# Optimization experiments

Hardware: AMD Instinct MI355X
Metric: run time of the kernel (lower is better)

The kernel has to match this reference:

```python
import jax, jax.numpy as jnp
import numpy as np
from jax import lax

B, T, A, L, H, FD = 32, 64, 6, 32, 128, 256


def setup_inputs() -> dict:
    key = jax.random.key(0)
    ks = jax.random.split(key, 24)
    rn = lambda k, s, sc: jax.random.normal(k, s, jnp.float32) * sc
    return {
        "states": rn(ks[0], (B, T, 3, 64, 64), 1.0),
        "actions": rn(ks[1], (B, T, A), 1.0),
        # CNN encoder params (scale ~ 1/sqrt(fan_in))
        "c1_w": rn(ks[2], (32, 3, 4, 4), 0.14), "c1_b": rn(ks[3], (32,), 0.01),
        "c2_w": rn(ks[4], (64, 32, 4, 4), 0.044), "c2_b": rn(ks[5], (64,), 0.01),
        "c3_w": rn(ks[6], (128, 64, 4, 4), 0.031), "c3_b": rn(ks[7], (128,), 0.01),
        "c4_w": rn(ks[8], (256, 128, 4, 4), 0.022), "c4_b": rn(ks[9], (256,), 0.01),
        "fc_w": rn(ks[10], (FD, 256 * 4 * 4), 0.0156), "fc_b": rn(ks[11], (FD,), 0.01),
        # GRUCell params (torch layout: W_ih (3H, in), W_hh (3H, H))
        "gru_wih": rn(ks[12], (3 * H, L + A), 0.16), "gru_whh": rn(ks[13], (3 * H, H), 0.088),
        "gru_bih": rn(ks[14], (3 * H,), 0.01), "gru_bhh": rn(ks[15], (3 * H,), 0.01),
        "prior_w": rn(ks[16], (2 * L, H), 0.088), "prior_b": rn(ks[17], (2 * L,), 0.01),
        "post_w": rn(ks[18], (2 * L, H + FD), 0.05), "post_b": rn(ks[19], (2 * L,), 0.01),
        # reparameterization noise (randn_like in torch), one per (b, t)
        "eps": rn(ks[20], (B, T, L), 1.0),
    }


def _conv(x, w, b):
    # Conv2d(k=4, stride=2, pad=1), NCHW/OIHW
    y = lax.conv_general_dilated(x, w, window_strides=(2, 2),
                                 padding=[(1, 1), (1, 1)],
                                 dimension_numbers=("NCHW", "OIHW", "NCHW"))
    return jax.nn.relu(y + b[None, :, None, None])


def _encode(x, c1_w, c1_b, c2_w, c2_b, c3_w, c3_b, c4_w, c4_b, fc_w, fc_b):
    # x: (N, 3, 64, 64) -> (N, FD)
    x = _conv(x, c1_w, c1_b)
    x = _conv(x, c2_w, c2_b)
    x = _conv(x, c3_w, c3_b)
    x = _conv(x, c4_w, c4_b)  # (N, 256, 4, 4)
    x = x.reshape(x.shape[0], -1)
    return x @ fc_w.T + fc_b


def _gru_cell(x, h, wih, whh, bih, bhh):
    gi = x @ wih.T + bih
    gh = h @ whh.T + bhh
    i_r, i_z, i_n = jnp.split(gi, 3, axis=-1)
    h_r, h_z, h_n = jnp.split(gh, 3, axis=-1)
    r = jax.nn.sigmoid(i_r + h_r)
    z = jax.nn.sigmoid(i_z + h_z)
    n = jnp.tanh(i_n + r * h_n)
    return (1.0 - z) * n + z * h


def reference(states, actions, c1_w, c1_b, c2_w, c2_b, c3_w, c3_b, c4_w, c4_b,
              fc_w, fc_b, gru_wih, gru_whh, gru_bih, gru_bhh,
              prior_w, prior_b, post_w, post_b, eps):
    b, t = states.shape[0], states.shape[1]
    # encoder has no recurrent dependency: encode all frames at once
    feats = _encode(states.reshape(b * t, *states.shape[2:]),
                    c1_w, c1_b, c2_w, c2_b, c3_w, c3_b, c4_w, c4_b,
                    fc_w, fc_b).reshape(b, t, -1)  # (B, T, FD)

    def step(carry, inp):
        h, z = carry
        a_t, f_t, e_t = inp
        h = _gru_cell(jnp.concatenate([z, a_t], -1), h,
                      gru_wih, gru_whh, gru_bih, gru_bhh)
        mu_p, lv_p = jnp.split(h @ prior_w.T + prior_b, 2, axis=-1)
        mu_q, lv_q = jnp.split(jnp.concatenate([h, f_t], -1) @ post_w.T + post_b, 2, axis=-1)
        z = mu_q + jnp.exp(0.5 * lv_q) * e_t
        return (h, z), (mu_p, lv_p, mu_q, lv_q, h, z)

    h0 = jnp.zeros((b, gru_whh.shape[1]), states.dtype)
    z0 = jnp.zeros((b, prior_w.shape[0] // 2), states.dtype)
    xs = (jnp.swapaxes(actions, 0, 1), jnp.swapaxes(feats, 0, 1),
          jnp.swapaxes(eps, 0, 1))
    _, ys = lax.scan(step, (h0, z0), xs)
    # (T, B, d) -> (B, T, d)
    return tuple(jnp.swapaxes(y, 0, 1) for y in ys)
```

## Files before the change

kernel.cpp:

```cpp
#include <hip/hip_runtime.h>
#include <math.h>

#define Bn 32
#define Tn 64
#define An 6
#define Ln 32
#define Hn 128
#define FDn 256
#define Nimg (Bn*Tn)

typedef __attribute__((ext_vector_type(8))) short frag_ab;
typedef __attribute__((ext_vector_type(4))) float frag_cd;
typedef _Float16 h2_t __attribute__((ext_vector_type(2)));

__device__ __forceinline__ float sigmoid_fast(float x){
  return __builtin_amdgcn_rcpf(1.f + __expf(-x));
}
__device__ __forceinline__ float tanh_fast(float x){
  float x2 = fminf(fmaxf(2.f*x, -30.f), 30.f);
  float e = __expf(x2);
  return (e - 1.f) * __builtin_amdgcn_rcpf(e + 1.f);
}

__device__ __forceinline__ unsigned short f2bf(float f){
  unsigned int u = __float_as_uint(f);
  unsigned int r = (u + 0x7fffu + ((u >> 16) & 1u)) >> 16;
  return (unsigned short)r;
}
__device__ __forceinline__ unsigned packh(float a, float b){
  union { h2_t h; unsigned u; } x;
  x.h = (h2_t){(_Float16)a, (_Float16)b};
  return x.u;
}
__device__ __forceinline__ float fdot2u(unsigned a, unsigned b, float c){
  union { unsigned u; h2_t h; } ua, ub;
  ua.u = a; ub.u = b;
#if __has_builtin(__builtin_amdgcn_fdot2)
  return __builtin_amdgcn_fdot2(ua.h, ub.h, c, false);
#else
  return c + (float)ua.h.x*(float)ub.h.x + (float)ua.h.y*(float)ub.h.y;
#endif
}
#define BAR_LDS() asm volatile("s_waitcnt lgkmcnt(0)\n\ts_barrier" ::: "memory")

__device__ __forceinline__ int swz_w(int r, int p){
  return ((r >> 4) << 9) + (p << 7) + ((((r & 15) ^ (p << 2))) << 3);
}
__device__ __forceinline__ int swz_r(int f, int l){
  return (f << 9) + ((l >> 4) << 7) + ((((l & 15) ^ ((l >> 4) << 2))) << 3);
}

__global__ void __launch_bounds__(256)
states_nhwc_kernel(const float* __restrict__ src, unsigned short* __restrict__ dst)
{
  int idx = blockIdx.x*256 + threadIdx.x;
  int n = idx >> 12, pix = idx & 4095;
  const float* s = src + (size_t)n*3*4096 + pix;
  union { unsigned short e[4]; uint2 v; } u;
  u.e[0] = f2bf(s[0]); u.e[1] = f2bf(s[4096]); u.e[2] = f2bf(s[8192]); u.e[3] = 0;
  *(uint2*)(dst + (size_t)idx*4) = u.v;
}

#define WHH4_U 24576
#define PO4_U  (64*53*4)
#define SCAN_U (WHH4_U + PO4_U)

__global__ void __launch_bounds__(256)
prep2_kernel(const float* __restrict__ c1w, const float* __restrict__ c2w,
             const float* __restrict__ c3w, const float* __restrict__ c4w,
             const float* __restrict__ fcw,
             const float* __restrict__ gwhh, const float* __restrict__ gwih,
             const float* __restrict__ prw,  const float* __restrict__ pow_,
             unsigned short* __restrict__ w1p, unsigned short* __restrict__ w2p,
             unsigned short* __restrict__ w3p, unsigned short* __restrict__ w4p,
             unsigned short* __restrict__ wfcp,
             unsigned* __restrict__ g_scan, unsigned* __restrict__ g_wih2,
             unsigned* __restrict__ g_pr2)
{
  const int bid = blockIdx.x, tid = threadIdx.x;
  if (bid < 128){
    int idx = bid*256+tid;
    int k = idx >> 9, r = idx & 511, tap = r >> 5, c = r & 31;
    w2p[idx] = f2bf(c2w[k*512 + c*16 + tap]);
  } else if (bid < 640){
    int idx = (bid-128)*256+tid;
    int k = idx >> 10, r = idx & 1023, tap = r >> 6, c = r & 63;
    w3p[idx] = f2bf(c3w[k*1024 + c*16 + tap]);
  } else if (bid < 2688){
    int idx = (bid-640)*256+tid;
    int k = idx >> 11, r = idx & 2047, tap = r >> 7, c = r & 127;
    w4p[idx] = f2bf(c4w[k*2048 + c*16 + tap]);
  } else if (bid < 6784){
    int idx = (bid-2688)*256+tid;
    int o = idx >> 12, r = idx & 4095, sp = r >> 8, c = r & 255;
    wfcp[idx] = f2bf(fcw[o*4096 + c*16 + sp]);
  } else if (bid < 6792){
    int idx = (bid-6784)*256+tid;
    int k = idx >> 6, r = idx & 63, tap = r >> 2, c = r & 3;
    w1p[idx] = (c < 3) ? f2bf(c1w[k*48 + c*16 + tap]) : (unsigned short)0;
  } else if (bid < 6888){
    int idx = (bid-6792)*256+tid;
    int q = idx & 3, r2 = idx >> 2;
    int k8 = r2 / 384, i = r2 - k8*384;
    int k = 8*k8 + 2*q;
    g_scan[idx] = packh(gwhh[i*128 + k], gwhh[i*128 + k + 1]);
  } else if (bid < 6917){
    int idx = (bid-6888)*256+tid;
    if (idx < 19*384){
      int c = idx / 384, i = idx - c*384;
      g_wih2[idx] = packh(gwih[i*38 + 2*c], gwih[i*38 + 2*c + 1]);
    }
  } else if (bid < 6933){
    int idx = (bid-6917)*256+tid;
    int o = idx >> 6, c = idx & 63;
    g_pr2[idx] = packh(prw[o*128 + 2*c], prw[o*128 + 2*c + 1]);
  } else {
    int idx = (bid-6933)*256+tid;
    if (idx < 64*192){
      int o = idx / 192, r2 = idx - o*192;
      int u = r2 >> 2, q = r2 & 3;
      int j = u / 12, kk = u - j*12;
      int k = 96*j + 8*kk + 2*q;
      g_scan[WHH4_U + (o*53 + j*13 + kk)*4 + q] =
        packh(pow_[o*384 + k], pow_[o*384 + k + 1]);
    }
  }
}

template<int Cin, int IN, int Kout, int OUT, int BN, int LOG_SPB>
__global__ void __launch_bounds__(256)
convN_mfma(const unsigned short* __restrict__ in,
           const unsigned short* __restrict__ wB,
           const float* __restrict__ bias,
           unsigned short* __restrict__ out)
{
  constexpr int SPB = OUT*OUT;
  constexpr int KD  = 16*Cin;
  constexpr int NCH = KD/32;
  constexpr int NFN = BN/32;
  constexpr int BFR = BN/16;
  constexpr int BSL = (BN*4 + 255)/256;
  __shared__ __align__(16) unsigned short Alds[2][8*512];
  __shared__ __align__(16) unsigned short Blds[2][BFR*512];

  const int tid = threadIdx.x;
  const int wave = tid >> 6, lane = tid & 63;
  const unsigned m0 = blockIdx.x * 128;
  const int n0 = blockIdx.y * BN;

  const int p = tid & 3;
  const unsigned short* baseA[2]; int oyA[2], oxA[2]; int AdstI[2];
#pragma unroll
  for (int h = 0; h < 2; h++){
    int r = (tid >> 2) + h*64;
    unsigned m = m0 + r;
    int nimg = m >> LOG_SPB;
    int sp = m & (SPB - 1);
    oyA[h] = sp / OUT; oxA[h] = sp & (OUT - 1);
    baseA[h] = in + (size_t)nimg * IN * IN * Cin;
    AdstI[h] = swz_w(r, p);
  }

  const unsigned short* BsrcH[BSL]; int BdstIH[BSL]; bool bActH[BSL];
#pragma unroll
  for (int h = 0; h < BSL; h++){
    int bn = (tid >> 2) + h*64, pb = tid & 3;
    bActH[h] = bn < BN;
    BsrcH[h] = wB + (size_t)(n0 + bn)*KD + pb*8;
    BdstIH[h] = swz_w(bn, pb);
  }

  const int mhalf = wave >> 1, nhalf = wave & 1;
  frag_cd acc[4][NFN];
#pragma unroll
  for (int i = 0; i < 4; i++)
#pragma unroll
    for (int j = 0; j < NFN; j++) acc[i][j] = (frag_cd){0.f,0.f,0.f,0.f};

  auto loadA = [&](int kt, int h) -> uint4 {
    if constexpr (Cin >= 32){
      constexpr int CPT = Cin/32;
      int tap = kt / CPT;
      int c0 = (kt - tap*CPT)*32;
      int kh = tap >> 2, kw = tap & 3;
      int iy = 2*oyA[h] - 1 + kh;
      int ix = 2*oxA[h] - 1 + kw;
      uint4 v = {0u,0u,0u,0u};
      if ((unsigned)iy < (unsigned)IN && (unsigned)ix < (unsigned)IN)
        v = *(const uint4*)(baseA[h] + ((iy*IN + ix)*Cin + c0 + p*8));
      return v;
    } else {
      int kh = kt*2 + (p >> 1);
      int kw0 = (p & 1)*2;
      int iy = 2*oyA[h] - 1 + kh;
      int ix0 = 2*oxA[h] - 1 + kw0;
      union { uint2 u2[2]; uint4 u4; } v; v.u4 = (uint4){0u,0u,0u,0u};
      bool iyok = (unsigned)iy < (unsigned)IN;
      const unsigned short* rowp = baseA[h] + iy*IN*4;
#pragma unroll
      for (int d = 0; d < 2; d++){
        int ix = ix0 + d;
        if (iyok && (unsigned)ix < (unsigned)IN) v.u2[d] = *(const uint2*)(rowp + ix*4);
      }
      return v.u4;
    }
  };

  const int rdoff = swz_r(0, lane);

  uint4 aR0 = loadA(0,0), aR1 = loadA(0,1);
  uint4 bR[BSL];
#pragma unroll
  for (int h = 0; h < BSL; h++)
    bR[h] = bActH[h] ? *(const uint4*)BsrcH[h] : (uint4){0u,0u,0u,0u};
  *(uint4*)&Alds[0][AdstI[0]] = aR0;
  *(uint4*)&Alds[0][AdstI[1]] = aR1;
#pragma unroll
  for (int h = 0; h < BSL; h++)
    if (bActH[h]) *(uint4*)&Blds[0][BdstIH[h]] = bR[h];
  if (NCH > 1){
    aR0 = loadA(1,0); aR1 = loadA(1,1);
#pragma unroll
    for (int h = 0; h < BSL; h++)
      if (bActH[h]) bR[h] = *(const uint4*)(BsrcH[h] + 32);
  }
  BAR_LDS();

#pragma unroll 2
  for (int kt = 0; kt < NCH; kt++){
    const int cur = kt & 1, nxt = cur ^ 1;
    if (kt + 1 < NCH){
      *(uint4*)&Alds[nxt][AdstI[0]] = aR0;
      *(uint4*)&Alds[nxt][AdstI[1]] = aR1;
#pragma unroll
      for (int h = 0; h < BSL; h++)
        if (bActH[h]) *(uint4*)&Blds[nxt][BdstIH[h]] = bR[h];
      if (kt + 2 < NCH){
        aR0 = loadA(kt+2, 0);
        aR1 = loadA(kt+2, 1);
#pragma unroll
        for (int h = 0; h < BSL; h++)
          if (bActH[h]) bR[h] = *(const uint4*)(BsrcH[h] + (kt+2)*32);
      }
    }
    frag_ab a[4], bf[NFN];
#pragma unroll
    for (int i = 0; i < 4; i++)
      a[i] = *(const frag_ab*)&Alds[cur][(((mhalf<<2) + i) << 9) + rdoff];
#pragma unroll
    for (int j = 0; j < NFN; j++)
      bf[j] = *(const frag_ab*)&Blds[cur][((nhalf*NFN + j) << 9) + rdoff];
#pragma unroll
    for (int i = 0; i < 4; i++)
#pragma unroll
      for (int j = 0; j < NFN; j++)
        acc[i][j] = __builtin_amdgcn_mfma_f32_16x16x32_bf16(a[i], bf[j], acc[i][j], 0, 0, 0);
    BAR_LDS();
  }

  const unsigned mb = m0 + mhalf*64 + ((lane >> 4) << 2);
#pragma unroll
  for (int j = 0; j < NFN; j++){
    const int kg = n0 + nhalf*(NFN*16) + j*16 + (lane & 15);
    const float bv = bias[kg];
#pragma unroll
    for (int i = 0; i < 4; i++){
#pragma unroll
      for (int r = 0; r < 4; r++){
        unsigned mg = mb + i*16 + r;
        out[(size_t)mg*Kout + kg] = f2bf(fmaxf(acc[i][j][r] + bv, 0.f));
      }
    }
  }
}

__global__ void __launch_bounds__(256)
fc_mfma2(const unsigned short* __restrict__ A, const unsigned short* __restrict__ wB,
         const float* __restrict__ bias, float* __restrict__ outF)
{
  constexpr int KD = 4096, NCH = KD/32;
  __shared__ __align__(16) unsigned short Alds[2][4*512];
  __shared__ __align__(16) unsigned short Blds[2][4*512];

  const int tid = threadIdx.x, wave = tid >> 6, lane = tid & 63;
  const int m0 = blockIdx.x * 64, n0 = blockIdx.y * 64;
  const int r = tid >> 2, pc = tid & 3;
  const unsigned short* Asrc = A + (size_t)(m0 + r)*KD + pc*8;
  const unsigned short* Bsrc = wB + (size_t)(n0 + r)*KD + pc*8;
  const int wI = swz_w(r, pc);
  const int mh = wave >> 1, nh = wave & 1;
  const int rdoff = swz_r(0, lane);

  frag_cd acc[2][2];
#pragma unroll
  for (int i = 0; i < 2; i++)
#pragma unroll
    for (int j = 0; j < 2; j++) acc[i][j] = (frag_cd){0.f,0.f,0.f,0.f};

  uint4 aP = *(const uint4*)Asrc, bP = *(const uint4*)Bsrc;
  *(uint4*)&Alds[0][wI] = aP;
  *(uint4*)&Blds[0][wI] = bP;
  aP = *(const uint4*)(Asrc + 32);
  bP = *(const uint4*)(Bsrc + 32);
  BAR_LDS();

#pragma unroll 2
  for (int kt = 0; kt < NCH; kt++){
    const int cur = kt & 1, nxt = cur ^ 1;
    if (kt + 1 < NCH){
      *(uint4*)&Alds[nxt][wI] = aP;
      *(uint4*)&Blds[nxt][wI] = bP;
      if (kt + 2 < NCH){
        aP = *(const uint4*)(Asrc + (kt+2)*32);
        bP = *(const uint4*)(Bsrc + (kt+2)*32);
      }
    }
    frag_ab a[2], b[2];
#pragma unroll
    for (int i = 0; i < 2; i++) a[i] = *(const frag_ab*)&Alds[cur][(((mh<<1)+i) << 9) + rdoff];
#pragma unroll
    for (int j = 0; j < 2; j++) b[j] = *(const frag_ab*)&Blds[cur][(((nh<<1)+j) << 9) + rdoff];
#pragma unroll
    for (int i = 0; i < 2; i++)
#pragma unroll
      for (int j = 0; j < 2; j++)
        acc[i][j] = __builtin_amdgcn_mfma_f32_16x16x32_bf16(a[i], b[j], acc[i][j], 0, 0, 0);
    BAR_LDS();
  }

  const int mb = m0 + mh*32 + ((lane >> 4) << 2);
#pragma unroll
  for (int j = 0; j < 2; j++){
    const int kg = n0 + nh*32 + j*16 + (lane & 15);
    const float bv = bias[kg];
#pragma unroll
    for (int i = 0; i < 2; i++)
#pragma unroll
      for (int rr = 0; rr < 4; rr++)
        outF[(size_t)(mb + i*16 + rr)*256 + kg] = acc[i][j][rr] + bv;
  }
}

__global__ void __launch_bounds__(384)
rssm_scan4(const float* __restrict__ actions, const float* __restrict__ feats,
           const float* __restrict__ eps,
           const unsigned* __restrict__ g_scan,
           const unsigned* __restrict__ g_wih2,
           const unsigned* __restrict__ g_pr2,
           const float* __restrict__ bih,  const float* __restrict__ bhh,
           const float* __restrict__ prior_b, const float* __restrict__ post_b,
           float* __restrict__ out)
{
  __shared__ __align__(16) _Float16 sh_hfh[384];
  __shared__ __align__(16) _Float16 sh_xh[40];
  __shared__ __align__(16) float sh_gi[384];
  __shared__ __align__(16) float sh_gh[384];

  const int b = blockIdx.x, tid = threadIdx.x;

  uint4 whhr[16];
  {
    const uint4* src = (const uint4*)g_scan;
#pragma unroll
    for (int k8 = 0; k8 < 16; k8++) whhr[k8] = src[k8*384 + tid];
  }
  unsigned wih[19];
#pragma unroll
  for (int c = 0; c < 19; c++) wih[c] = g_wih2[c*384 + tid];

  unsigned prw[32];
  float prb = 0.f;
  if (tid < 128){
    const unsigned* src = g_pr2 + (tid >> 1)*64 + (tid & 1)*32;
#pragma unroll
    for (int c = 0; c < 32; c++) prw[c] = src[c];
    prb = prior_b[tid >> 1];
  }

  int om = 0, pj = 0, o_p = 0; bool is_mu = false; float pob = 0.f;
  uint4 pww[12];
  if (tid >= 128){
    const int tt = tid - 128;
    om = tt >> 2; pj = tt & 3;
    o_p = (om >> 1) + (om & 1)*32;
    is_mu = !(om & 1);
    pob = post_b[o_p];
    const uint4* src = (const uint4*)(g_scan + WHH4_U) + o_p*53 + pj*13;
#pragma unroll
    for (int kk = 0; kk < 12; kk++) pww[kk] = src[kk];
  }

  const float bih_i = bih[tid], bhh_i = bhh[tid];
  float hreg = 0.f;

  {
    const int bt0 = b*Tn;
    if (tid < Hn) sh_hfh[tid] = (_Float16)0.f;
    if (tid < Ln) sh_xh[tid] = (_Float16)0.f;
    if (tid >= 32 && tid < 38) sh_xh[tid] = (_Float16)actions[(size_t)bt0*An + (tid-32)];
    if (tid >= 64 && tid < 320) sh_hfh[128 + tid - 64] = (_Float16)feats[(size_t)bt0*FDn + (tid-64)];
  }
  __syncthreads();

  const uint4* H4   = (const uint4*)sh_hfh;
  const unsigned* X2 = (const unsigned*)sh_xh;

  const int OFF_MUP = 0;
  const int OFF_LVP = Bn*Tn*Ln;
  const int OFF_MUQ = 2*Bn*Tn*Ln;
  const int OFF_LVQ = 3*Bn*Tn*Ln;
  const int OFF_H   = 4*Bn*Tn*Ln;
  const int OFF_Z   = 4*Bn*Tn*Ln + Bn*Tn*Hn;

  float freg = 0.f, areg = 0.f, epsr = 0.f;

  for (int t = 0; t < Tn; t++){
    const int bt = b*Tn + t;

    if (t > 0 && tid >= 64 && tid < 320) sh_hfh[128 + tid - 64] = (_Float16)freg;
    if (t < Tn-1){
      if (tid >= 64 && tid < 320) freg = feats[(size_t)(bt+1)*FDn + (tid-64)];
      if (tid >= 320 && tid < 326) areg = actions[(size_t)(bt+1)*An + (tid-320)];
    }
    if (tid >= 128 && ((tid-128)&7) == 0) epsr = eps[(size_t)bt*Ln + ((tid-128)>>3)];

    {
      float a0 = bih_i, a1 = 0.f;
#pragma unroll
      for (int c = 0; c < 19; c += 2) a0 = fdot2u(wih[c], X2[c], a0);
#pragma unroll
      for (int c = 1; c < 19; c += 2) a1 = fdot2u(wih[c], X2[c], a1);
      sh_gi[tid] = a0 + a1;

      float g0 = bhh_i, g1 = 0.f, g2 = 0.f, g3 = 0.f;
#pragma unroll
      for (int k8 = 0; k8 < 16; k8++){
        uint4 w = whhr[k8];
        uint4 h = H4[k8];
        g0 = fdot2u(w.x, h.x, g0);
        g1 = fdot2u(w.y, h.y, g1);
        g2 = fdot2u(w.z, h.z, g2);
        g3 = fdot2u(w.w, h.w, g3);
      }
      sh_gh[tid] = (g0 + g1) + (g2 + g3);
    }
    BAR_LDS();

    if (tid < Hn){
      const float r  = sigmoid_fast(sh_gi[tid]       + sh_gh[tid]);
      const float zg = sigmoid_fast(sh_gi[Hn  + tid] + sh_gh[Hn  + tid]);
      const float nn = tanh_fast(fmaf(r, sh_gh[2*Hn + tid], sh_gi[2*Hn + tid]));
      hreg = (1.f - zg)*nn + zg*hreg;
      sh_hfh[tid] = (_Float16)hreg;
      out[OFF_H + (size_t)bt*Hn + tid] = hreg;
    }
    if (t < Tn-1 && tid >= 320 && tid < 326) sh_xh[32 + tid - 320] = (_Float16)areg;
    BAR_LDS();

    if (tid < 128){
      const int j = tid & 1;
      float a0 = 0.f, a1 = 0.f, a2 = 0.f, a3 = 0.f;
#pragma unroll
      for (int c4 = 0; c4 < 8; c4++){
        uint4 h = H4[8*j + c4];
        a0 = fdot2u(prw[4*c4+0], h.x, a0);
        a1 = fdot2u(prw[4*c4+1], h.y, a1);
        a2 = fdot2u(prw[4*c4+2], h.z, a2);
        a3 = fdot2u(prw[4*c4+3], h.w, a3);
      }
      float p = (a0 + a1) + (a2 + a3);
      p += __shfl_xor(p, 1);
      if (j == 0){
        const int o = tid >> 1;
        p += prb;
        if (o < Ln) out[OFF_MUP + (size_t)bt*Ln + o] = p;
        else        out[OFF_LVP + (size_t)bt*Ln + (o - Ln)] = p;
      }
    } else {
      float a0 = 0.f, a1 = 0.f, a2 = 0.f, a3 = 0.f;
#pragma unroll
      for (int kk = 0; kk < 12; kk++){
        uint4 w = pww[kk];
        uint4 h = H4[pj*12 + kk];
        a0 = fdot2u(w.x, h.x, a0);
        a1 = fdot2u(w.y, h.y, a1);
        a2 = fdot2u(w.z, h.z, a2);
        a3 = fdot2u(w.w, h.w, a3);
      }
      float p = (a0 + a1) + (a2 + a3);
      p += __shfl_xor(p, 1);
      p += __shfl_xor(p, 2);
      p += pob;
      const float q_part = __shfl_xor(p, 4);
      if (pj == 0){
        if (is_mu){
          const int o = om >> 1;
          out[OFF_MUQ + (size_t)bt*Ln + o] = p;
          const float zz = fmaf(__expf(0.5f*q_part), epsr, p);
          sh_xh[o] = (_Float16)zz;
          out[OFF_Z + (size_t)bt*Ln + o] = zz;
        } else {
          out[OFF_LVQ + (size_t)bt*Ln + (o_p - Ln)] = p;
        }
      }
    }
    BAR_LDS();
  }
}

extern "C" void kernel_launch(void* const* d_in, const int* in_sizes, int n_in,
                              void* d_out, int out_size, void* d_ws, size_t ws_size,
                              hipStream_t stream)
{
  const float* states = (const float*)d_in[0];
  const float* actions= (const float*)d_in[1];
  const float* c1_w = (const float*)d_in[2];  const float* c1_b = (const float*)d_in[3];
  const float* c2_w = (const float*)d_in[4];  const float* c2_b = (const float*)d_in[5];
  const float* c3_w = (const float*)d_in[6];  const float* c3_b = (const float*)d_in[7];
  const float* c4_w = (const float*)d_in[8];  const float* c4_b = (const float*)d_in[9];
  const float* fc_w = (const float*)d_in[10]; const float* fc_b = (const float*)d_in[11];
  const float* gwih = (const float*)d_in[12]; const float* gwhh = (const float*)d_in[13];
  const float* gbih = (const float*)d_in[14]; const float* gbhh = (const float*)d_in[15];
  const float* pr_w = (const float*)d_in[16]; const float* pr_b = (const float*)d_in[17];
  const float* po_w = (const float*)d_in[18]; const float* po_b = (const float*)d_in[19];
  const float* eps  = (const float*)d_in[20];

  char* p = (char*)d_ws;
  auto alloc = [&](size_t bytes){ char* r = p; p += (bytes + 255) & ~255ULL; return r; };

  unsigned short* statesB = (unsigned short*)alloc((size_t)Nimg*4096*4*2);
  unsigned short* act1    = (unsigned short*)alloc((size_t)Nimg*1024*32*2);
  unsigned short* act2    = (unsigned short*)alloc((size_t)Nimg*256*64*2);
  unsigned short* act3    = (unsigned short*)alloc((size_t)Nimg*64*128*2);
  unsigned short* act4    = (unsigned short*)alloc((size_t)Nimg*16*256*2);
  float*          feats   = (float*)alloc((size_t)Nimg*FDn*4);
  unsigned short* w1p     = (unsigned short*)alloc(32*64*2);
  unsigned short* w2p     = (unsigned short*)alloc((size_t)64*512*2);
  unsigned short* w3p     = (unsigned short*)alloc((size_t)128*1024*2);
  unsigned short* w4p     = (unsigned short*)alloc((size_t)256*2048*2);
  unsigned short* wfcp    = (unsigned short*)alloc((size_t)256*4096*2);
  unsigned* g_scan = (unsigned*)alloc((size_t)SCAN_U*4);
  unsigned* g_wih2 = (unsigned*)alloc((size_t)19*384*4);
  unsigned* g_pr2  = (unsigned*)alloc((size_t)64*64*4);

  states_nhwc_kernel<<<Nimg*4096/256, 256, 0, stream>>>(states, statesB);
  prep2_kernel<<<6981, 256, 0, stream>>>(c1_w, c2_w, c3_w, c4_w, fc_w,
                                         gwhh, gwih, pr_w, po_w,
                                         w1p, w2p, w3p, w4p, wfcp,
                                         g_scan, g_wih2, g_pr2);

  convN_mfma<4,64,32,32,32,10>  <<< dim3(Nimg*1024/128, 1), 256, 0, stream >>>(statesB, w1p, c1_b, act1);
  convN_mfma<32,32,64,16,64,8>  <<< dim3(Nimg*256/128, 1), 256, 0, stream >>>(act1, w2p, c2_b, act2);
  convN_mfma<64,16,128,8,128,6> <<< dim3(Nimg*64/128, 1), 256, 0, stream >>>(act2, w3p, c3_b, act3);
  convN_mfma<128,8,256,4,128,4> <<< dim3(Nimg*16/128, 2), 256, 0, stream >>>(act3, w4p, c4_b, act4);

  fc_mfma2<<< dim3(Nimg/64, 4), 256, 0, stream >>>(act4, wfcp, fc_b, feats);

  rssm_scan4<<< Bn, 384, 0, stream >>>(actions, feats, eps,
                                       g_scan, g_wih2, g_pr2,
                                       gbih, gbhh, pr_b, po_b, (float*)d_out);
}
```

Baseline: 564.4 us.

## Batch RSSM scan over 16 sequences per block using f16 MFMA

Replaces the per-sequence scalar fdot2 recurrent scan (32 blocks of 384 threads) with an MFMA-based scan in which each of 2 blocks handles 16 batch rows, computing GRU, prior and posterior matmuls as 16x16x32 f16 MFMAs. Precomputes the action contribution plus biases (GIA), transposes eps, and packs feats into MFMA fragment layout in separate prep kernels. The intent is to cut the serial per-step latency of the scan by using matrix cores and amortising weight registers across 16 sequences. In exchange only 2 CUs are used, extra prep kernels and global buffers are added, and the per-step critical path now has three barriers plus MFMA latency chains.

```diff
diff --git a/kernel.cpp b/kernel.cpp
--- a/kernel.cpp
+++ b/kernel.cpp
@@ -11,7 +11,7 @@
 
 typedef __attribute__((ext_vector_type(8))) short frag_ab;
 typedef __attribute__((ext_vector_type(4))) float frag_cd;
-typedef _Float16 h2_t __attribute__((ext_vector_type(2)));
+typedef __attribute__((ext_vector_type(8))) _Float16 frag_h;
 
 __device__ __forceinline__ float sigmoid_fast(float x){
   return __builtin_amdgcn_rcpf(1.f + __expf(-x));
@@ -27,19 +27,8 @@
   unsigned int r = (u + 0x7fffu + ((u >> 16) & 1u)) >> 16;
   return (unsigned short)r;
 }
-__device__ __forceinline__ unsigned packh(float a, float b){
-  union { h2_t h; unsigned u; } x;
-  x.h = (h2_t){(_Float16)a, (_Float16)b};
-  return x.u;
-}
-__device__ __forceinline__ float fdot2u(unsigned a, unsigned b, float c){
-  union { unsigned u; h2_t h; } ua, ub;
-  ua.u = a; ub.u = b;
-#if __has_builtin(__builtin_amdgcn_fdot2)
-  return __builtin_amdgcn_fdot2(ua.h, ub.h, c, false);
-#else
-  return c + (float)ua.h.x*(float)ub.h.x + (float)ua.h.y*(float)ub.h.y;
-#endif
+__device__ __forceinline__ unsigned short f2h(float f){
+  union { _Float16 h; unsigned short u; } x; x.h = (_Float16)f; return x.u;
 }
 #define BAR_LDS() asm volatile("s_waitcnt lgkmcnt(0)\n\ts_barrier" ::: "memory")
 
@@ -61,21 +50,20 @@
   *(uint2*)(dst + (size_t)idx*4) = u.v;
 }
 
-#define WHH4_U 24576
-#define PO4_U  (64*53*4)
-#define SCAN_U (WHH4_U + PO4_U)
-
 __global__ void __launch_bounds__(256)
 prep2_kernel(const float* __restrict__ c1w, const float* __restrict__ c2w,
              const float* __restrict__ c3w, const float* __restrict__ c4w,
              const float* __restrict__ fcw,
              const float* __restrict__ gwhh, const float* __restrict__ gwih,
              const float* __restrict__ prw,  const float* __restrict__ pow_,
+             const float* __restrict__ actions, const float* __restrict__ bih,
+             const float* __restrict__ bhh,  const float* __restrict__ eps,
              unsigned short* __restrict__ w1p, unsigned short* __restrict__ w2p,
              unsigned short* __restrict__ w3p, unsigned short* __restrict__ w4p,
              unsigned short* __restrict__ wfcp,
-             unsigned* __restrict__ g_scan, unsigned* __restrict__ g_wih2,
-             unsigned* __restrict__ g_pr2)
+             unsigned short* __restrict__ gWhh, unsigned short* __restrict__ gWz,
+             unsigned short* __restrict__ gWpo, unsigned short* __restrict__ gWpr,
+             float* __restrict__ GIA, float* __restrict__ gEps)
 {
   const int bid = blockIdx.x, tid = threadIdx.x;
   if (bid < 128){
@@ -98,33 +86,52 @@
     int idx = (bid-6784)*256+tid;
     int k = idx >> 6, r = idx & 63, tap = r >> 2, c = r & 3;
     w1p[idx] = (c < 3) ? f2bf(c1w[k*48 + c*16 + tap]) : (unsigned short)0;
-  } else if (bid < 6888){
+  } else if (bid < 6984){
     int idx = (bid-6792)*256+tid;
-    int q = idx & 3, r2 = idx >> 2;
-    int k8 = r2 / 384, i = r2 - k8*384;
-    int k = 8*k8 + 2*q;
-    g_scan[idx] = packh(gwhh[i*128 + k], gwhh[i*128 + k + 1]);
-  } else if (bid < 6917){
-    int idx = (bid-6888)*256+tid;
-    if (idx < 19*384){
-      int c = idx / 384, i = idx - c*384;
-      g_wih2[idx] = packh(gwih[i*38 + 2*c], gwih[i*38 + 2*c + 1]);
-    }
-  } else if (bid < 6933){
-    int idx = (bid-6917)*256+tid;
-    int o = idx >> 6, c = idx & 63;
-    g_pr2[idx] = packh(prw[o*128 + 2*c], prw[o*128 + 2*c + 1]);
+    int nt = idx >> 11, kt = (idx >> 9) & 3;
+    int li = (idx >> 3) & 63, j = idx & 7;
+    gWhh[idx] = f2h(gwhh[(nt*16 + (li&15))*128 + (kt<<5) + ((li>>4)<<3) + j]);
+  } else if (bid < 7032){
+    int idx = (bid-6984)*256+tid;
+    int nt = idx >> 9, li = (idx >> 3) & 63, j = idx & 7;
+    gWz[idx] = f2h(gwih[(nt*16 + (li&15))*38 + ((li>>4)<<3) + j]);
+  } else if (bid < 7128){
+    int idx = (bid-7032)*256+tid;
+    int nt = idx / 6144, rem = idx % 6144, kt = rem >> 9;
+    int li = (idx >> 3) & 63, j = idx & 7;
+    gWpo[idx] = f2h(pow_[(nt*16 + (li&15))*384 + (kt<<5) + ((li>>4)<<3) + j]);
+  } else if (bid < 7160){
+    int idx = (bid-7128)*256+tid;
+    int nt = idx >> 11, kt = (idx >> 9) & 3;
+    int li = (idx >> 3) & 63, j = idx & 7;
+    gWpr[idx] = f2h(prw[(nt*16 + (li&15))*128 + (kt<<5) + ((li>>4)<<3) + j]);
+  } else if (bid < 10232){
+    int idx = (bid-7160)*256+tid;
+    int m = idx & 15, q = idx >> 4;
+    int n = q % 384, q2 = q / 384;
+    int t = q2 & 63, g = q2 >> 6;
+    int b = g*16 + m;
+    float v = bih[n] + (n < 256 ? bhh[n] : 0.f);
+    const float* ar = actions + ((size_t)b*64 + t)*6;
+    const float* wr = gwih + n*38 + 32;
+#pragma unroll
+    for (int k = 0; k < 6; k++) v += ar[k] * wr[k];
+    GIA[idx] = v;
   } else {
-    int idx = (bid-6933)*256+tid;
-    if (idx < 64*192){
-      int o = idx / 192, r2 = idx - o*192;
-      int u = r2 >> 2, q = r2 & 3;
-      int j = u / 12, kk = u - j*12;
-      int k = 96*j + 8*kk + 2*q;
-      g_scan[WHH4_U + (o*53 + j*13 + kk)*4 + q] =
-        packh(pow_[o*384 + k], pow_[o*384 + k + 1]);
-    }
-  }
+    int idx = (bid-10232)*256+tid;
+    int m = idx & 15, o = (idx >> 4) & 31, t = (idx >> 9) & 63, g = idx >> 15;
+    gEps[idx] = eps[((size_t)(g*16 + m)*64 + t)*32 + o];
+  }
+}
+
+__global__ void __launch_bounds__(256)
+feats_pack(const float* __restrict__ feats, unsigned short* __restrict__ gF)
+{
+  int idx = blockIdx.x*256 + threadIdx.x;
+  int j = idx & 7, li = (idx >> 3) & 63, kt = (idx >> 9) & 7;
+  int t = (idx >> 12) & 63, g = idx >> 18;
+  int r = li & 15, k = ((li >> 4) << 3) + j;
+  gF[idx] = f2h(feats[(size_t)((g*16 + r)*64 + t)*256 + (kt<<5) + k]);
 }
 
 template<int Cin, int IN, int Kout, int OUT, int BN, int LOG_SPB>
@@ -341,69 +348,35 @@
   }
 }
 
-__global__ void __launch_bounds__(384)
-rssm_scan4(const float* __restrict__ actions, const float* __restrict__ feats,
-           const float* __restrict__ eps,
-           const unsigned* __restrict__ g_scan,
-           const unsigned* __restrict__ g_wih2,
-           const unsigned* __restrict__ g_pr2,
-           const float* __restrict__ bih,  const float* __restrict__ bhh,
-           const float* __restrict__ prior_b, const float* __restrict__ post_b,
-           float* __restrict__ out)
+__global__ void __launch_bounds__(512, 2)
+rssm_mfma(const unsigned short* __restrict__ gWhh,
+          const unsigned short* __restrict__ gWz,
+          const unsigned short* __restrict__ gWpo,
+          const unsigned short* __restrict__ gWpr,
+          const unsigned short* __restrict__ gF,
+          const float* __restrict__ GIA,
+          const float* __restrict__ gEps,
+          const float* __restrict__ bhh,
+          const float* __restrict__ pr_b,
+          const float* __restrict__ po_b,
+          float* __restrict__ out)
 {
-  __shared__ __align__(16) _Float16 sh_hfh[384];
-  __shared__ __align__(16) _Float16 sh_xh[40];
-  __shared__ __align__(16) float sh_gi[384];
-  __shared__ __align__(16) float sh_gh[384];
-
-  const int b = blockIdx.x, tid = threadIdx.x;
-
-  uint4 whhr[16];
-  {
-    const uint4* src = (const uint4*)g_scan;
-#pragma unroll
-    for (int k8 = 0; k8 < 16; k8++) whhr[k8] = src[k8*384 + tid];
-  }
-  unsigned wih[19];
-#pragma unroll
-  for (int c = 0; c < 19; c++) wih[c] = g_wih2[c*384 + tid];
-
-  unsigned prw[32];
-  float prb = 0.f;
-  if (tid < 128){
-    const unsigned* src = g_pr2 + (tid >> 1)*64 + (tid & 1)*32;
-#pragma unroll
-    for (int c = 0; c < 32; c++) prw[c] = src[c];
-    prb = prior_b[tid >> 1];
-  }
-
-  int om = 0, pj = 0, o_p = 0; bool is_mu = false; float pob = 0.f;
-  uint4 pww[12];
-  if (tid >= 128){
-    const int tt = tid - 128;
-    om = tt >> 2; pj = tt & 3;
-    o_p = (om >> 1) + (om & 1)*32;
-    is_mu = !(om & 1);
-    pob = post_b[o_p];
-    const uint4* src = (const uint4*)(g_scan + WHH4_U) + o_p*53 + pj*13;
-#pragma unroll
-    for (int kk = 0; kk < 12; kk++) pww[kk] = src[kk];
-  }
-
-  const float bih_i = bih[tid], bhh_i = bhh[tid];
-  float hreg = 0.f;
-
-  {
-    const int bt0 = b*Tn;
-    if (tid < Hn) sh_hfh[tid] = (_Float16)0.f;
-    if (tid < Ln) sh_xh[tid] = (_Float16)0.f;
-    if (tid >= 32 && tid < 38) sh_xh[tid] = (_Float16)actions[(size_t)bt0*An + (tid-32)];
-    if (tid >= 64 && tid < 320) sh_hfh[128 + tid - 64] = (_Float16)feats[(size_t)bt0*FDn + (tid-64)];
-  }
-  __syncthreads();
-
-  const uint4* H4   = (const uint4*)sh_hfh;
-  const unsigned* X2 = (const unsigned*)sh_xh;
+  __shared__ __align__(16) unsigned short Hlds[4*512];
+  __shared__ __align__(16) unsigned short Zlds[512];
+  __shared__ __align__(16) float Ssum[16*256];
+  __shared__ __align__(16) float Gin[16*128];
+  __shared__ __align__(16) float Ghn[16*128];
+
+  const int g = blockIdx.x, tid = threadIdx.x;
+  const int wv = tid >> 6, lane = tid & 63;
+  const int dn = lane & 15, dm4 = (lane >> 4) << 2;
+  const int l8 = lane << 3;
+  const int rdoff = swz_r(0, lane);
+
+  const int gm = tid & 15;
+  const int gj = (tid >> 4) << 2;
+  const int gxm = (gm & 7) << 2;
+  const int hws = ((gj >> 5) << 9) + swz_w(gm, (gj & 31) >> 3) + (gj & 7);
 
   const int OFF_MUP = 0;
   const int OFF_LVP = Bn*Tn*Ln;
@@ -412,99 +385,218 @@
   const int OFF_H   = 4*Bn*Tn*Ln;
   const int OFF_Z   = 4*Bn*Tn*Ln + Bn*Tn*Hn;
 
-  float freg = 0.f, areg = 0.f, epsr = 0.f;
-
-  for (int t = 0; t < Tn; t++){
-    const int bt = b*Tn + t;
-
-    if (t > 0 && tid >= 64 && tid < 320) sh_hfh[128 + tid - 64] = (_Float16)freg;
-    if (t < Tn-1){
-      if (tid >= 64 && tid < 320) freg = feats[(size_t)(bt+1)*FDn + (tid-64)];
-      if (tid >= 320 && tid < 326) areg = actions[(size_t)(bt+1)*An + (tid-320)];
-    }
-    if (tid >= 128 && ((tid-128)&7) == 0) epsr = eps[(size_t)bt*Ln + ((tid-128)>>3)];
-
-    {
-      float a0 = bih_i, a1 = 0.f;
-#pragma unroll
-      for (int c = 0; c < 19; c += 2) a0 = fdot2u(wih[c], X2[c], a0);
-#pragma unroll
-      for (int c = 1; c < 19; c += 2) a1 = fdot2u(wih[c], X2[c], a1);
-      sh_gi[tid] = a0 + a1;
-
-      float g0 = bhh_i, g1 = 0.f, g2 = 0.f, g3 = 0.f;
-#pragma unroll
-      for (int k8 = 0; k8 < 16; k8++){
-        uint4 w = whhr[k8];
-        uint4 h = H4[k8];
-        g0 = fdot2u(w.x, h.x, g0);
-        g1 = fdot2u(w.y, h.y, g1);
-        g2 = fdot2u(w.z, h.z, g2);
-        g3 = fdot2u(w.w, h.w, g3);
-      }
-      sh_gh[tid] = (g0 + g1) + (g2 + g3);
-    }
+  ((uint2*)Hlds)[tid] = (uint2){0u,0u};
+  if (tid < 128) ((uint2*)Zlds)[tid] = (uint2){0u,0u};
+
+  float h_old[4] = {0.f,0.f,0.f,0.f};
+
+  auto do_gates = [&](int t) {
+    const int xr = gj ^ gxm;
+    frag_cd vr = *(const frag_cd*)&Ssum[(gm<<8) + xr];
+    frag_cd vz = *(const frag_cd*)&Ssum[(gm<<8) + 128 + xr];
+    frag_cd vi = *(const frag_cd*)&Gin[(gm<<7) + xr];
+    frag_cd vh = *(const frag_cd*)&Ghn[(gm<<7) + xr];
+    float hnew[4];
+#pragma unroll
+    for (int q = 0; q < 4; q++){
+      float rr = sigmoid_fast(vr[q]);
+      float zz = sigmoid_fast(vz[q]);
+      float nn = tanh_fast(fmaf(rr, vh[q], vi[q]));
+      hnew[q] = (1.f - zz)*nn + zz*h_old[q];
+      h_old[q] = hnew[q];
+    }
+    union { _Float16 h[4]; uint2 u; } hw;
+#pragma unroll
+    for (int q = 0; q < 4; q++) hw.h[q] = (_Float16)hnew[q];
+    *(uint2*)&Hlds[hws] = hw.u;
+    *(float4*)(out + OFF_H + (size_t)((g*16 + gm)*64 + t)*128 + gj) =
+        (float4){hnew[0],hnew[1],hnew[2],hnew[3]};
+  };
+
+  if (wv < 6){
+    frag_h Bhh[4][4], Bz[4];
+    const int nt0 = wv << 2;
+#pragma unroll
+    for (int nt = 0; nt < 4; nt++){
+#pragma unroll
+      for (int kt = 0; kt < 4; kt++)
+        Bhh[nt][kt] = *(const frag_h*)(gWhh + ((((nt0+nt)<<2) + kt)<<9) + l8);
+      Bz[nt] = *(const frag_h*)(gWz + ((nt0+nt)<<9) + l8);
+    }
+    frag_h Bpr[2][4]; float prb2[2] = {0.f,0.f};
+    if (wv < 2){
+#pragma unroll
+      for (int i = 0; i < 2; i++){
+        int nt = (wv<<1) + i;
+#pragma unroll
+        for (int kt = 0; kt < 4; kt++)
+          Bpr[i][kt] = *(const frag_h*)(gWpr + (((nt<<2)+kt)<<9) + l8);
+        prb2[i] = pr_b[(nt<<4) + dn];
+      }
+    }
+    float bhh4[4] = {0.f,0.f,0.f,0.f};
+    if (wv >= 4){
+#pragma unroll
+      for (int nt = 0; nt < 4; nt++)
+        bhh4[nt] = bhh[256 + ((wv-4)<<6) + (nt<<4) + dn];
+    }
+    frag_cd giaP[4];
+#pragma unroll
+    for (int nt = 0; nt < 4; nt++)
+      giaP[nt] = *(const frag_cd*)(GIA + ((size_t)(g*64)*384 + (wv<<6) + (nt<<4) + dn)*16 + dm4);
     BAR_LDS();
 
-    if (tid < Hn){
-      const float r  = sigmoid_fast(sh_gi[tid]       + sh_gh[tid]);
-      const float zg = sigmoid_fast(sh_gi[Hn  + tid] + sh_gh[Hn  + tid]);
-      const float nn = tanh_fast(fmaf(r, sh_gh[2*Hn + tid], sh_gi[2*Hn + tid]));
-      hreg = (1.f - zg)*nn + zg*hreg;
-      sh_hfh[tid] = (_Float16)hreg;
-      out[OFF_H + (size_t)bt*Hn + tid] = hreg;
-    }
-    if (t < Tn-1 && tid >= 320 && tid < 326) sh_xh[32 + tid - 320] = (_Float16)areg;
+    for (int t = 0; t < Tn; t++){
+      frag_h hA[4], zA;
+      zA = *(const frag_h*)&Zlds[rdoff];
+#pragma unroll
+      for (int kt = 0; kt < 4; kt++)
+        hA[kt] = *(const frag_h*)&Hlds[(kt<<9) + rdoff];
+      if (wv < 4){
+        frag_cd acc[4];
+#pragma unroll
+        for (int nt = 0; nt < 4; nt++){
+          acc[nt] = giaP[nt];
+          acc[nt] = __builtin_amdgcn_mfma_f32_16x16x32_f16(zA, Bz[nt], acc[nt], 0,0,0);
+        }
+#pragma unroll
+        for (int kt = 0; kt < 4; kt++)
+#pragma unroll
+          for (int nt = 0; nt < 4; nt++)
+            acc[nt] = __builtin_amdgcn_mfma_f32_16x16x32_f16(hA[kt], Bhh[nt][kt], acc[nt], 0,0,0);
+#pragma unroll
+        for (int nt = 0; nt < 4; nt++){
+          const int n = (wv<<6) + (nt<<4) + dn;
+#pragma unroll
+          for (int r = 0; r < 4; r++){
+            const int m = dm4 + r;
+            Ssum[(m<<8) + (n ^ ((m&7)<<2))] = acc[nt][r];
+          }
+        }
+      } else {
+        frag_cd ai[4], ah[4];
+#pragma unroll
+        for (int nt = 0; nt < 4; nt++){
+          ai[nt] = giaP[nt];
+          ai[nt] = __builtin_amdgcn_mfma_f32_16x16x32_f16(zA, Bz[nt], ai[nt], 0,0,0);
+          ah[nt] = (frag_cd){bhh4[nt],bhh4[nt],bhh4[nt],bhh4[nt]};
+        }
+#pragma unroll
+        for (int kt = 0; kt < 4; kt++)
+#pragma unroll
+          for (int nt = 0; nt < 4; nt++)
+            ah[nt] = __builtin_amdgcn_mfma_f32_16x16x32_f16(hA[kt], Bhh[nt][kt], ah[nt], 0,0,0);
+#pragma unroll
+        for (int nt = 0; nt < 4; nt++){
+          const int jj = ((wv-4)<<6) + (nt<<4) + dn;
+#pragma unroll
+          for (int r = 0; r < 4; r++){
+            const int m = dm4 + r;
+            const int x = jj ^ ((m&7)<<2);
+            Gin[(m<<7) + x] = ai[nt][r];
+            Ghn[(m<<7) + x] = ah[nt][r];
+          }
+        }
+      }
+      BAR_LDS();
+
+      if (t < Tn-1){
+#pragma unroll
+        for (int nt = 0; nt < 4; nt++)
+          giaP[nt] = *(const frag_cd*)(GIA + ((size_t)(g*64 + t+1)*384 + (wv<<6) + (nt<<4) + dn)*16 + dm4);
+      }
+      do_gates(t);
+      BAR_LDS();
+
+      if (wv < 2){
+        frag_h hB[4];
+#pragma unroll
+        for (int kt = 0; kt < 4; kt++)
+          hB[kt] = *(const frag_h*)&Hlds[(kt<<9) + rdoff];
+        frag_cd ap[2];
+#pragma unroll
+        for (int i = 0; i < 2; i++) ap[i] = (frag_cd){prb2[i],prb2[i],prb2[i],prb2[i]};
+#pragma unroll
+        for (int kt = 0; kt < 4; kt++)
+#pragma unroll
+          for (int i = 0; i < 2; i++)
+            ap[i] = __builtin_amdgcn_mfma_f32_16x16x32_f16(hB[kt], Bpr[i][kt], ap[i], 0,0,0);
+#pragma unroll
+        for (int i = 0; i < 2; i++){
+          const int o = ((wv<<1)+i)*16 + dn;
+#pragma unroll
+          for (int r = 0; r < 4; r++){
+            const size_t bt = (size_t)(g*16 + dm4 + r)*64 + t;
+            if (wv == 0) out[OFF_MUP + bt*32 + o] = ap[i][r];
+            else         out[OFF_LVP + bt*32 + (o-32)] = ap[i][r];
+          }
+        }
+      }
+      BAR_LDS();
+    }
+  } else {
+    const int ow = wv - 6;
+    frag_h Bpo[2][12];
+#pragma unroll
+    for (int i = 0; i < 2; i++){
+      const int nt = ow + (i<<1);
+#pragma unroll
+      for (int kt = 0; kt < 12; kt++)
+        Bpo[i][kt] = *(const frag_h*)(gWpo + ((nt*12 + kt)<<9) + l8);
+    }
+    float pob2[2];
+#pragma unroll
+    for (int i = 0; i < 2; i++) pob2[i] = po_b[(ow + (i<<1))*16 + dn];
+    const int oo = (ow<<4) + dn;
+    frag_h Ff[8];
+#pragma unroll
+    for (int kt = 0; kt < 8; kt++)
+      Ff[kt] = *(const frag_h*)(gF + ((size_t)((g*64)*8 + kt)<<9) + l8);
+    float4 epsP = *(const float4*)(gEps + ((size_t)(g*64)*32 + oo)*16 + dm4);
     BAR_LDS();
 
-    if (tid < 128){
-      const int j = tid & 1;
-      float a0 = 0.f, a1 = 0.f, a2 = 0.f, a3 = 0.f;
-#pragma unroll
-      for (int c4 = 0; c4 < 8; c4++){
-        uint4 h = H4[8*j + c4];
-        a0 = fdot2u(prw[4*c4+0], h.x, a0);
-        a1 = fdot2u(prw[4*c4+1], h.y, a1);
-        a2 = fdot2u(prw[4*c4+2], h.z, a2);
-        a3 = fdot2u(prw[4*c4+3], h.w, a3);
-      }
-      float p = (a0 + a1) + (a2 + a3);
-      p += __shfl_xor(p, 1);
-      if (j == 0){
-        const int o = tid >> 1;
-        p += prb;
-        if (o < Ln) out[OFF_MUP + (size_t)bt*Ln + o] = p;
-        else        out[OFF_LVP + (size_t)bt*Ln + (o - Ln)] = p;
-      }
-    } else {
-      float a0 = 0.f, a1 = 0.f, a2 = 0.f, a3 = 0.f;
-#pragma unroll
-      for (int kk = 0; kk < 12; kk++){
-        uint4 w = pww[kk];
-        uint4 h = H4[pj*12 + kk];
-        a0 = fdot2u(w.x, h.x, a0);
-        a1 = fdot2u(w.y, h.y, a1);
-        a2 = fdot2u(w.z, h.z, a2);
-        a3 = fdot2u(w.w, h.w, a3);
-      }
-      float p = (a0 + a1) + (a2 + a3);
-      p += __shfl_xor(p, 1);
-      p += __shfl_xor(p, 2);
-      p += pob;
-      const float q_part = __shfl_xor(p, 4);
-      if (pj == 0){
-        if (is_mu){
-          const int o = om >> 1;
-          out[OFF_MUQ + (size_t)bt*Ln + o] = p;
-          const float zz = fmaf(__expf(0.5f*q_part), epsr, p);
-          sh_xh[o] = (_Float16)zz;
-          out[OFF_Z + (size_t)bt*Ln + o] = zz;
-        } else {
-          out[OFF_LVQ + (size_t)bt*Ln + (o_p - Ln)] = p;
-        }
-      }
-    }
-    BAR_LDS();
+    for (int t = 0; t < Tn; t++){
+      frag_cd pacc[2];
+#pragma unroll
+      for (int i = 0; i < 2; i++) pacc[i] = (frag_cd){pob2[i],pob2[i],pob2[i],pob2[i]};
+#pragma unroll
+      for (int kt = 0; kt < 8; kt++)
+#pragma unroll
+        for (int i = 0; i < 2; i++)
+          pacc[i] = __builtin_amdgcn_mfma_f32_16x16x32_f16(Ff[kt], Bpo[i][4+kt], pacc[i], 0,0,0);
+      BAR_LDS();
+
+      if (t < Tn-1){
+#pragma unroll
+        for (int kt = 0; kt < 8; kt++)
+          Ff[kt] = *(const frag_h*)(gF + ((size_t)((g*64 + t+1)*8 + kt)<<9) + l8);
+      }
+      do_gates(t);
+      BAR_LDS();
+
+      frag_h hB[4];
+#pragma unroll
+      for (int kt = 0; kt < 4; kt++)
+        hB[kt] = *(const frag_h*)&Hlds[(kt<<9) + rdoff];
+#pragma unroll
+      for (int kt = 0; kt < 4; kt++)
+#pragma unroll
+        for (int i = 0; i < 2; i++)
+          pacc[i] = __builtin_amdgcn_mfma_f32_16x16x32_f16(hB[kt], Bpo[i][kt], pacc[i], 0,0,0);
+#pragma unroll
+      for (int r = 0; r < 4; r++){
+        const size_t bt = (size_t)(g*16 + dm4 + r)*64 + t;
+        const float mu = pacc[0][r], lv = pacc[1][r];
+        out[OFF_MUQ + bt*32 + oo] = mu;
+        out[OFF_LVQ + bt*32 + oo] = lv;
+        const float zz = fmaf(__expf(0.5f*lv), (&epsP.x)[r], mu);
+        out[OFF_Z + bt*32 + oo] = zz;
+        Zlds[swz_w(dm4 + r, oo>>3) + (oo&7)] = f2h(zz);
+      }
+      if (t < Tn-1)
+        epsP = *(const float4*)(gEps + ((size_t)(g*64 + t+1)*32 + oo)*16 + dm4);
+      BAR_LDS();
+    }
   }
 }
 
@@ -539,15 +631,20 @@
   unsigned short* w3p     = (unsigned short*)alloc((size_t)128*1024*2);
   unsigned short* w4p     = (unsigned short*)alloc((size_t)256*2048*2);
   unsigned short* wfcp    = (unsigned short*)alloc((size_t)256*4096*2);
-  unsigned* g_scan = (unsigned*)alloc((size_t)SCAN_U*4);
-  unsigned* g_wih2 = (unsigned*)alloc((size_t)19*384*4);
-  unsigned* g_pr2  = (unsigned*)alloc((size_t)64*64*4);
+  unsigned short* gWhhp   = (unsigned short*)alloc((size_t)49152*2);
+  unsigned short* gWzp    = (unsigned short*)alloc((size_t)12288*2);
+  unsigned short* gWpop   = (unsigned short*)alloc((size_t)24576*2);
+  unsigned short* gWprp   = (unsigned short*)alloc((size_t)8192*2);
+  unsigned short* gFA     = (unsigned short*)alloc((size_t)524288*2);
+  float*          GIAb    = (float*)alloc((size_t)786432*4);
+  float*          gEpsb   = (float*)alloc((size_t)65536*4);
 
   states_nhwc_kernel<<<Nimg*4096/256, 256, 0, stream>>>(states, statesB);
-  prep2_kernel<<<6981, 256, 0, stream>>>(c1_w, c2_w, c3_w, c4_w, fc_w,
-                                         gwhh, gwih, pr_w, po_w,
-                                         w1p, w2p, w3p, w4p, wfcp,
-                                         g_scan, g_wih2, g_pr2);
+  prep2_kernel<<<10488, 256, 0, stream>>>(c1_w, c2_w, c3_w, c4_w, fc_w,
+                                          gwhh, gwih, pr_w, po_w,
+                                          actions, gbih, gbhh, eps,
+                                          w1p, w2p, w3p, w4p, wfcp,
+                                          gWhhp, gWzp, gWpop, gWprp, GIAb, gEpsb);
 
   convN_mfma<4,64,32,32,32,10>  <<< dim3(Nimg*1024/128, 1), 256, 0, stream >>>(statesB, w1p, c1_b, act1);
   convN_mfma<32,32,64,16,64,8>  <<< dim3(Nimg*256/128, 1), 256, 0, stream >>>(act1, w2p, c2_b, act2);
@@ -555,8 +652,8 @@
   convN_mfma<128,8,256,4,128,4> <<< dim3(Nimg*16/128, 2), 256, 0, stream >>>(act3, w4p, c4_b, act4);
 
   fc_mfma2<<< dim3(Nimg/64, 4), 256, 0, stream >>>(act4, wfcp, fc_b, feats);
-
-  rssm_scan4<<< Bn, 384, 0, stream >>>(actions, feats, eps,
-                                       g_scan, g_wih2, g_pr2,
-                                       gbih, gbhh, pr_b, po_b, (float*)d_out);
-}
+  feats_pack<<< 2048, 256, 0, stream >>>(feats, gFA);
+
+  rssm_mfma<<< 2, 512, 0, stream >>>(gWhhp, gWzp, gWpop, gWprp, gFA,
+                                     GIAb, gEpsb, gbhh, pr_b, po_b, (float*)d_out);
+}
```

New measurement: 588.7 us. 1.04x slower.
